# Kernel optimization log

Hardware: AMD Instinct MI355X
Metric: run time of the kernel (lower is better)

Reference implementation:

```python
import jax, jax.numpy as jnp
import numpy as np

B, L, D, H = 2, 2048, 1024, 16
HD = D // H


def setup_inputs() -> dict:
    key = jax.random.key(0)
    ks = jax.random.split(key, 14)
    s = 0.02
    return {
        "hidden_states": jax.random.normal(ks[0], (B, L, D), jnp.float32),
        "position_embeddings": jax.random.normal(ks[1], (B, L, D), jnp.float32),
        "Wcq": jax.random.normal(ks[2], (D, D), jnp.float32) * s,
        "bcq": jnp.zeros((D,), jnp.float32),
        "Wck": jax.random.normal(ks[3], (D, D), jnp.float32) * s,
        "bck": jnp.zeros((D,), jnp.float32),
        "Wpq": jax.random.normal(ks[4], (D, D), jnp.float32) * s,
        "bpq": jnp.zeros((D,), jnp.float32),
        "Wpk": jax.random.normal(ks[5], (D, D), jnp.float32) * s,
        "bpk": jnp.zeros((D,), jnp.float32),
        "rel_bias": jnp.zeros((1, H, 1, 1), jnp.float32),
        "Wo": jax.random.normal(ks[6], (D, D), jnp.float32) * s,
        "bo": jnp.zeros((D,), jnp.float32),
    }


def _split_heads(x):
    # [B, L, D] -> [B, H, L, HD]
    b, l, _ = x.shape
    return x.reshape(b, l, H, HD).transpose(0, 2, 1, 3)


def reference(hidden_states, position_embeddings, Wcq, bcq, Wck, bck,
              Wpq, bpq, Wpk, bpk, rel_bias, Wo, bo):
    cq = _split_heads(hidden_states @ Wcq + bcq)
    ck = _split_heads(hidden_states @ Wck + bck)
    # NOTE: original code (faithfully reproduced) uses content_key as the value
    cv = ck
    pq = _split_heads(position_embeddings @ Wpq + bpq)
    pk = _split_heads(position_embeddings @ Wpk + bpk)

    scores = (jnp.einsum("bhqd,bhkd->bhqk", cq, ck)
              + jnp.einsum("bhqd,bhkd->bhqk", pq, pk)
              + rel_bias)
    attn_weights = jax.nn.softmax(scores / jnp.sqrt(jnp.float32(HD)), axis=-1)
    ctx = jnp.einsum("bhqk,bhkd->bhqd", attn_weights, cv)
    ctx = ctx.transpose(0, 2, 1, 3).reshape(hidden_states.shape[0], -1, D)
    output = ctx @ Wo + bo
    return output, attn_weights
```

## Files before the change

kernel.cpp:

```cpp
#include <hip/hip_runtime.h>
#include <hip/hip_bf16.h>
#include <math.h>


#define Bc 2
#define Lc 2048
#define Dc 1024
#define Hc 16
#define Mc (Bc*Lc)
#define NT 32

typedef __attribute__((ext_vector_type(8))) __bf16 bf16x8;
typedef __attribute__((ext_vector_type(4))) float f32x4;
typedef __attribute__((ext_vector_type(16))) float f32x16;
typedef __attribute__((ext_vector_type(2))) unsigned u32x2;

union U4 { unsigned u[4]; bf16x8 v; };

__device__ __forceinline__ void gl_lds16(const void* g, void* l) {
    __builtin_amdgcn_global_load_lds(
        (const __attribute__((address_space(1))) void*)g,
        (__attribute__((address_space(3))) void*)l, 16, 0, 0);
}
__device__ __forceinline__ unsigned pkbf(float a, float b) {
    unsigned short ua = __builtin_bit_cast(unsigned short, (__bf16)a);
    unsigned short ub = __builtin_bit_cast(unsigned short, (__bf16)b);
    return (unsigned)ua | ((unsigned)ub << 16);
}
__device__ __forceinline__ float lo2f(unsigned u){ return __builtin_bit_cast(float, u << 16); }
__device__ __forceinline__ float hi2f(unsigned u){ return __builtin_bit_cast(float, u & 0xffff0000u); }
#define E2(x) __builtin_amdgcn_exp2f(x)

#define WAIT_VM0  asm volatile("s_waitcnt vmcnt(0)" ::: "memory")
#define WAIT_VM4  asm volatile("s_waitcnt vmcnt(4)" ::: "memory")
#define WAIT_VM8  asm volatile("s_waitcnt vmcnt(8)" ::: "memory")
#define WAIT_VM12 asm volatile("s_waitcnt vmcnt(12)" ::: "memory")
#define WAIT_LG0  asm volatile("s_waitcnt lgkmcnt(0)" ::: "memory")
#define SBAR __builtin_amdgcn_sched_barrier(0)
#define BARRIER do { __builtin_amdgcn_sched_barrier(0); __builtin_amdgcn_s_barrier(); __builtin_amdgcn_sched_barrier(0); } while (0)

__global__ __launch_bounds__(256) void prep_kernel(
    const float* __restrict__ Wcq, const float* __restrict__ Wck,
    const float* __restrict__ Wpq, const float* __restrict__ Wpk,
    const float* __restrict__ Wo,
    __bf16* __restrict__ Wt, __bf16* __restrict__ Woh, __bf16* __restrict__ Wol)
{
    const int z = blockIdx.z;
    const float* W = (z==0)?Wcq:(z==1)?Wck:(z==2)?Wpq:(z==3)?Wpk:Wo;
    const int t = threadIdx.x;
    const int n  = blockIdx.x*64 + (t & 63);
    const int k0 = blockIdx.y*128 + (t >> 6)*32;
    float v[32];
    #pragma unroll
    for (int j = 0; j < 32; ++j) v[j] = W[(size_t)(k0+j)*Dc + n];
    if (z < 4) {
        __bf16* dst = Wt + (size_t)z*Dc*Dc + (size_t)n*Dc + k0;
        #pragma unroll
        for (int c = 0; c < 4; ++c) {
            bf16x8 o;
            #pragma unroll
            for (int j = 0; j < 8; ++j) o[j] = (__bf16)v[c*8+j];
            *(bf16x8*)(dst + c*8) = o;
        }
    } else {
        __bf16* dh = Woh + (size_t)n*Dc + k0;
        __bf16* dl = Wol + (size_t)n*Dc + k0;
        #pragma unroll
        for (int c = 0; c < 4; ++c) {
            bf16x8 oh, ol;
            #pragma unroll
            for (int j = 0; j < 8; ++j) {
                float x = v[c*8+j];
                __bf16 hi = (__bf16)x;
                oh[j] = hi; ol[j] = (__bf16)(x - (float)hi);
            }
            *(bf16x8*)(dh + c*8) = oh;
            *(bf16x8*)(dl + c*8) = ol;
        }
    }
}

__global__ __launch_bounds__(256) void proj_kernel(
    const float* __restrict__ hidden, const float* __restrict__ pos,
    const __bf16* __restrict__ Wt,
    const float* __restrict__ bcq, const float* __restrict__ bck,
    const float* __restrict__ bpq, const float* __restrict__ bpk,
    __bf16* __restrict__ Qc, __bf16* __restrict__ Kc)
{
    const int g = blockIdx.x;
    const int nblk = g >> 7, sg = g & 127, mblk = sg & 31, z = sg >> 5;
    const int m0 = mblk*128, n0 = nblk*128;
    const float* X = (z < 2) ? hidden : pos;
    const __bf16* Wz = Wt + (size_t)z*Dc*Dc;
    const float* bias = (z==0)?bcq:(z==1)?bck:(z==2)?bpq:bpk;
    __bf16* dst = (z & 1) ? Kc : Qc;
    const int half = z >> 1;
    const float scale = (z & 1) ? 1.0f : 0.18033688011112042f;

    const int t = threadIdx.x, lane = t & 63, w = t >> 6;
    const int wm = w >> 1, wn = w & 1;

    __shared__ __align__(16) float  Asf[128][32];
    __shared__ __align__(16) __bf16 Bs[128][32];

    const int arowL = lane >> 3;
    const int acol  = ((lane & 7) ^ arowL) * 4;
    const int brow4 = lane >> 2;
    const int bcol  = ((lane & 3) ^ (brow4 & 3)) * 8;

    f32x4 acc[4][4] = {};

    for (int k0 = 0; k0 < Dc; k0 += 32) {
        #pragma unroll
        for (int i = 0; i < 4; ++i) {
            int row = 8*(4*w+i) + arowL;
            gl_lds16(X + (size_t)(m0+row)*Dc + k0 + acol, (char*)Asf + (4*w+i)*1024);
        }
        #pragma unroll
        for (int i = 0; i < 2; ++i) {
            int row = 16*(2*w+i) + brow4;
            gl_lds16(Wz + (size_t)(n0+row)*Dc + k0 + bcol, (char*)Bs + (2*w+i)*1024);
        }
        WAIT_VM0; __syncthreads();
        bf16x8 a[4], b[4];
        const int s2 = lane >> 4;
        #pragma unroll
        for (int i = 0; i < 4; ++i) {
            int R = wm*64 + i*16 + (lane&15);
            f32x4 x0 = *(const f32x4*)((const char*)&Asf[R][0] + (((2*s2  ) ^ (R&7))*16));
            f32x4 x1 = *(const f32x4*)((const char*)&Asf[R][0] + (((2*s2+1) ^ (R&7))*16));
            bf16x8 af;
            af[0]=(__bf16)x0[0]; af[1]=(__bf16)x0[1]; af[2]=(__bf16)x0[2]; af[3]=(__bf16)x0[3];
            af[4]=(__bf16)x1[0]; af[5]=(__bf16)x1[1]; af[6]=(__bf16)x1[2]; af[7]=(__bf16)x1[3];
            a[i] = af;
            int Rb = wn*64 + i*16 + (lane&15);
            b[i] = *(const bf16x8*)((const char*)&Bs[Rb][0] + ((s2 ^ (Rb&3))*16));
        }
        #pragma unroll
        for (int mi = 0; mi < 4; ++mi)
            #pragma unroll
            for (int ni = 0; ni < 4; ++ni)
                acc[mi][ni] = __builtin_amdgcn_mfma_f32_16x16x32_bf16(a[mi], b[ni], acc[mi][ni], 0, 0, 0);
        __syncthreads();
    }
    #pragma unroll
    for (int mi = 0; mi < 4; ++mi)
        #pragma unroll
        for (int ni = 0; ni < 4; ++ni)
            #pragma unroll
            for (int r = 0; r < 4; ++r) {
                int row = m0 + wm*64 + mi*16 + (lane>>4)*4 + r;
                int col = n0 + wn*64 + ni*16 + (lane&15);
                float v = (acc[mi][ni][r] + bias[col]) * scale;
                int bb = row >> 11, l = row & (Lc-1);
                int hh = col >> 6,  hd = col & 63;
                dst[(((size_t)bb*Hc + hh)*Lc + l)*128 + half*64 + hd] = (__bf16)v;
            }
}

__global__ __launch_bounds__(256) void vt_kernel(
    const __bf16* __restrict__ Kc, __bf16* __restrict__ VT)
{
    const int l0 = blockIdx.x * 128, hb = blockIdx.y;
    const int t = threadIdx.x, w = t >> 6, lane = t & 63;
    __shared__ __bf16 T[128][72];
    const __bf16* src = Kc + ((size_t)hb*Lc + l0)*128;
    {
        const int lr = t >> 3, cc = t & 7;
        #pragma unroll
        for (int j = 0; j < 4; ++j)
            *(bf16x8*)&T[lr + j*32][cc*8] = *(const bf16x8*)(src + (size_t)(lr + j*32)*128 + cc*8);
    }
    __syncthreads();
    {
        const int d = lane;
        __bf16* dstp = VT + ((size_t)hb*64 + d)*Lc + l0 + w*32;
        #pragma unroll
        for (int j = 0; j < 4; ++j) {
            bf16x8 o;
            #pragma unroll
            for (int i = 0; i < 8; ++i) o[i] = T[w*32 + j*8 + i][d];
            *(bf16x8*)(dstp + j*8) = o;
        }
    }
}

__global__ __launch_bounds__(256, 2) void attn1_kernel(
    const __bf16* __restrict__ Qc, const __bf16* __restrict__ Kc,
    const float* __restrict__ rel_bias, float* __restrict__ baddp)
{
    const int g = blockIdx.x;
    const int qt = g >> 5, hb = g & 31, h = hb & 15;
    const int q0 = qt * 128;
    const int t = threadIdx.x, lane = t & 63, w = t >> 6;
    const int ln31 = lane & 31, hi = lane >> 5;

    const __bf16* Qp = Qc + (size_t)hb * Lc * 128;
    const __bf16* Kp = Kc + (size_t)hb * Lc * 128;

    __shared__ __align__(16) char smem[49152];

    bf16x8 qa[8];
    {
        const __bf16* qrow = Qp + (size_t)(q0 + w*32 + ln31) * 128 + hi*8;
        #pragma unroll
        for (int ks = 0; ks < 8; ++ks) qa[ks] = *(const bf16x8*)(qrow + ks*16);
    }

    int kof[4];
    #pragma unroll
    for (int c = 0; c < 4; ++c) {
        int rl = c*4 + (lane >> 4);
        int rr = w*16 + rl;
        kof[c] = rr*128 + (((lane & 15) ^ rl) * 8);
    }
    int kR[8];
    #pragma unroll
    for (int ks = 0; ks < 8; ++ks) kR[ks] = ((ks*2 + hi) ^ (lane & 15)) * 8;

    #define STAGE_K(B, KT) do { \
        const __bf16* kb_ = Kp + (size_t)(KT)*8192; \
        gl_lds16(kb_ + kof[0], smem + ((B)*64 + w*16 +  0)*256); \
        gl_lds16(kb_ + kof[1], smem + ((B)*64 + w*16 +  4)*256); \
        gl_lds16(kb_ + kof[2], smem + ((B)*64 + w*16 +  8)*256); \
        gl_lds16(kb_ + kof[3], smem + ((B)*64 + w*16 + 12)*256); \
    } while (0)
    #define KB(B, ROW, KS) (*(const bf16x8*)(smem + ((B)*64 + (ROW))*256 + kR[KS]*2))

    const float bc = rel_bias[h] * 0.18033688011112042f;
    float lp[4] = {0.f, 0.f, 0.f, 0.f};

    STAGE_K(0, 0); STAGE_K(1, 1);
    WAIT_VM4; BARRIER;
    for (int kt = 0; kt < NT; ++kt) {
        if (kt+2 < NT) STAGE_K((kt+2) % 3, kt+2);
        SBAR;
        const int buf = kt % 3;
        f32x16 s0, s1;
        #pragma unroll
        for (int r = 0; r < 16; ++r) { s0[r] = bc; s1[r] = bc; }
        __builtin_amdgcn_s_setprio(1);
        #pragma unroll
        for (int ks = 0; ks < 8; ++ks) {
            bf16x8 kb0 = KB(buf, ln31, ks);
            bf16x8 kb1 = KB(buf, 32 + ln31, ks);
            s0 = __builtin_amdgcn_mfma_f32_32x32x16_bf16(kb0, qa[ks], s0, 0, 0, 0);
            s1 = __builtin_amdgcn_mfma_f32_32x32x16_bf16(kb1, qa[ks], s1, 0, 0, 0);
        }
        __builtin_amdgcn_s_setprio(0);
        #pragma unroll
        for (int r = 0; r < 16; ++r) {
            lp[r & 3] += E2(s0[r]);
            lp[r & 3] += E2(s1[r]);
        }
        if (kt+2 < NT) { WAIT_VM4; } else { WAIT_VM0; }
        BARRIER;
    }
    float lsum = (lp[0] + lp[1]) + (lp[2] + lp[3]);
    lsum += __shfl_xor(lsum, 32);
    if (!hi) baddp[(size_t)hb*Lc + q0 + w*32 + ln31] = bc - log2f(lsum);
    #undef STAGE_K
    #undef KB
}

__global__ __launch_bounds__(256, 2) void attn2_kernel(
    const __bf16* __restrict__ Qc, const __bf16* __restrict__ Kc,
    const __bf16* __restrict__ VT, const float* __restrict__ baddp,
    float* __restrict__ attn, __bf16* __restrict__ ctxh)
{
    const int g = blockIdx.x;
    const int qt = g >> 5, hb = g & 31, h = hb & 15, bb = hb >> 4;
    const int q0 = qt * 128;
    const int t = threadIdx.x, lane = t & 63, w = t >> 6;
    const int ln31 = lane & 31, hi = lane >> 5;

    const __bf16* Qp = Qc + (size_t)hb * Lc * 128;
    const __bf16* Kp = Kc + (size_t)hb * Lc * 128;
    const __bf16* Vp = VT + (size_t)hb * 64 * Lc;

    __shared__ __align__(16) char smem[81920];
    char* const VsB = smem + 49152;
    char* const PsW = smem + 65536 + w*4096;

    bf16x8 qa[8];
    {
        const __bf16* qrow = Qp + (size_t)(q0 + w*32 + ln31) * 128 + hi*8;
        #pragma unroll
        for (int ks = 0; ks < 8; ++ks) qa[ks] = *(const bf16x8*)(qrow + ks*16);
    }
    const float badd = baddp[(size_t)hb*Lc + q0 + w*32 + ln31];

    int kof[4];
    #pragma unroll
    for (int c = 0; c < 4; ++c) {
        int rl = c*4 + (lane >> 4);
        int rr = w*16 + rl;
        kof[c] = rr*128 + (((lane & 15) ^ rl) * 8);
    }
    int vof[2];
    #pragma unroll
    for (int c = 0; c < 2; ++c) {
        int dl = lane >> 3;
        int dd = w*16 + c*8 + dl;
        vof[c] = dd*2048 + (((lane & 7) ^ dl) * 8);
    }
    int kR[8];
    #pragma unroll
    for (int ks = 0; ks < 8; ++ks) kR[ks] = ((ks*2 + hi) ^ (lane & 15)) * 8;
    int vR[4];
    #pragma unroll
    for (int ks = 0; ks < 4; ++ks) vR[ks] = ((ks*2 + hi) ^ (lane & 7)) * 8;

    #define STAGE_K(B, KT) do { \
        const __bf16* kb_ = Kp + (size_t)(KT)*8192; \
        gl_lds16(kb_ + kof[0], smem + ((B)*64 + w*16 +  0)*256); \
        gl_lds16(kb_ + kof[1], smem + ((B)*64 + w*16 +  4)*256); \
        gl_lds16(kb_ + kof[2], smem + ((B)*64 + w*16 +  8)*256); \
        gl_lds16(kb_ + kof[3], smem + ((B)*64 + w*16 + 12)*256); \
    } while (0)
    #define STAGE_V(B, KT) do { \
        const __bf16* vb_ = Vp + (KT)*64; \
        gl_lds16(vb_ + vof[0], VsB + ((B)*64 + w*16 + 0)*128); \
        gl_lds16(vb_ + vof[1], VsB + ((B)*64 + w*16 + 8)*128); \
    } while (0)
    #define KB(B, ROW, KS) (*(const bf16x8*)(smem + ((B)*64 + (ROW))*256 + kR[KS]*2))
    #define VB(B, ROW, KS) (*(const bf16x8*)(VsB  + ((B)*64 + (ROW))*128 + vR[KS]*2))

    f32x16 ctx0 = {}, ctx1 = {};
    float* abase = attn + ((size_t)hb*Lc + q0 + w*32)*Lc;
    const int rr2 = lane >> 4;
    const int s8  = lane & 15;

    STAGE_K(0, 0); STAGE_V(0, 0); STAGE_K(1, 1);
    WAIT_VM4; BARRIER;

    for (int kt = 0; kt < NT; ++kt) {
        if (kt+1 < NT) STAGE_V((kt+1) & 1, kt+1);
        if (kt+2 < NT) STAGE_K((kt+2) % 3, kt+2);
        SBAR;
        const int buf = kt % 3;
        f32x16 s0, s1;
        #pragma unroll
        for (int r = 0; r < 16; ++r) { s0[r] = badd; s1[r] = badd; }
        __builtin_amdgcn_s_setprio(1);
        #pragma unroll
        for (int ks = 0; ks < 8; ++ks) {
            bf16x8 kb0 = KB(buf, ln31, ks);
            bf16x8 kb1 = KB(buf, 32 + ln31, ks);
            s0 = __builtin_amdgcn_mfma_f32_32x32x16_bf16(kb0, qa[ks], s0, 0, 0, 0);
            s1 = __builtin_amdgcn_mfma_f32_32x32x16_bf16(kb1, qa[ks], s1, 0, 0, 0);
        }
        __builtin_amdgcn_s_setprio(0);
        unsigned u0[8], u1[8], r0[8], r1[8];
        #pragma unroll
        for (int gq = 0; gq < 4; ++gq) {
            u0[gq]   = pkbf(E2(s0[4*gq+0]), E2(s0[4*gq+1]));
            u1[gq]   = pkbf(E2(s0[4*gq+2]), E2(s0[4*gq+3]));
            u0[4+gq] = pkbf(E2(s1[4*gq+0]), E2(s1[4*gq+1]));
            u1[4+gq] = pkbf(E2(s1[4*gq+2]), E2(s1[4*gq+3]));
        }
        #pragma unroll
        for (int gq = 0; gq < 8; ++gq) {
            r0[gq] = __shfl_xor(u0[gq], 32);
            r1[gq] = __shfl_xor(u1[gq], 32);
        }
        bf16x8 pb[4];
        #pragma unroll
        for (int ks = 0; ks < 4; ++ks) {
            const int gq = 2*ks + hi;
            U4 u;
            u.u[0] = hi ? r0[gq] : u0[gq];
            u.u[1] = hi ? r1[gq] : u1[gq];
            u.u[2] = hi ? u0[gq] : r0[gq];
            u.u[3] = hi ? u1[gq] : r1[gq];
            pb[ks] = u.v;
            *(bf16x8*)(PsW + ln31*128 + ((gq ^ (ln31 & 7))*16)) = u.v;
        }
        __builtin_amdgcn_s_setprio(1);
        #pragma unroll
        for (int ks = 0; ks < 4; ++ks) {
            bf16x8 v0 = VB(kt & 1, ln31, ks);
            bf16x8 v1 = VB(kt & 1, 32 + ln31, ks);
            ctx0 = __builtin_amdgcn_mfma_f32_32x32x16_bf16(pb[ks], v0, ctx0, 0, 0, 0);
            ctx1 = __builtin_amdgcn_mfma_f32_32x32x16_bf16(pb[ks], v1, ctx1, 0, 0, 0);
        }
        __builtin_amdgcn_s_setprio(0);
        WAIT_LG0; SBAR;
        #pragma unroll
        for (int j = 0; j < 8; ++j) {
            const int row = j*4 + rr2;
            u32x2 d = *(const u32x2*)(PsW + row*128 + (((s8>>1) ^ (row&7))*16) + (s8&1)*8);
            f32x4 o;
            o[0]=lo2f(d[0]); o[1]=hi2f(d[0]); o[2]=lo2f(d[1]); o[3]=hi2f(d[1]);
            __builtin_nontemporal_store(o, (f32x4*)(abase + (size_t)row*Lc + kt*64 + s8*4));
        }
        if (kt+1 < NT) {
            if (kt+2 < NT) { WAIT_VM12; } else { WAIT_VM8; }
            BARRIER;
        }
    }

    #pragma unroll
    for (int r = 0; r < 16; ++r) {
        const int R = (r&3) + 8*(r>>2) + 4*hi;
        const size_t row = (size_t)bb*Lc + q0 + w*32 + R;
        ctxh[row*Dc + h*64 + ln31]      = (__bf16)ctx0[r];
        ctxh[row*Dc + h*64 + 32 + ln31] = (__bf16)ctx1[r];
    }
    #undef STAGE_K
    #undef STAGE_V
    #undef KB
    #undef VB
}

__global__ __launch_bounds__(256) void out_kernel(
    const __bf16* __restrict__ ctxh, const __bf16* __restrict__ Woh,
    const __bf16* __restrict__ Wol, const float* __restrict__ bo,
    float* __restrict__ out)
{
    const int m0 = blockIdx.y * 128, n0 = blockIdx.x * 128;
    const int t = threadIdx.x, lane = t & 63, w = t >> 6;
    const int wm = w >> 1, wn = w & 1;

    __shared__ __align__(16) __bf16 As[128][32];
    __shared__ __align__(16) __bf16 Bh[128][32];
    __shared__ __align__(16) __bf16 Bl[128][32];

    const int row4 = lane >> 2;
    const int scol = ((lane & 3) ^ (row4 & 3)) * 8;

    f32x4 acc[4][4] = {};

    for (int k0 = 0; k0 < Dc; k0 += 32) {
        #pragma unroll
        for (int i = 0; i < 2; ++i) {
            int row = 16*(2*w+i) + row4;
            gl_lds16(ctxh + (size_t)(m0+row)*Dc + k0 + scol, (char*)As + (2*w+i)*1024);
            gl_lds16(Woh  + (size_t)(n0+row)*Dc + k0 + scol, (char*)Bh + (2*w+i)*1024);
            gl_lds16(Wol  + (size_t)(n0+row)*Dc + k0 + scol, (char*)Bl + (2*w+i)*1024);
        }
        WAIT_VM0; __syncthreads();
        bf16x8 a[4], bh[4], bl[4];
        const int s2 = lane >> 4;
        #pragma unroll
        for (int i = 0; i < 4; ++i) {
            int Ra = wm*64 + i*16 + (lane&15);
            int Rb = wn*64 + i*16 + (lane&15);
            a[i]  = *(const bf16x8*)((const char*)&As[Ra][0] + ((s2 ^ (Ra&3))*16));
            bh[i] = *(const bf16x8*)((const char*)&Bh[Rb][0] + ((s2 ^ (Rb&3))*16));
            bl[i] = *(const bf16x8*)((const char*)&Bl[Rb][0] + ((s2 ^ (Rb&3))*16));
        }
        #pragma unroll
        for (int mi = 0; mi < 4; ++mi)
            #pragma unroll
            for (int ni = 0; ni < 4; ++ni) {
                acc[mi][ni] = __builtin_amdgcn_mfma_f32_16x16x32_bf16(a[mi], bh[ni], acc[mi][ni], 0, 0, 0);
                acc[mi][ni] = __builtin_amdgcn_mfma_f32_16x16x32_bf16(a[mi], bl[ni], acc[mi][ni], 0, 0, 0);
            }
        __syncthreads();
    }
    #pragma unroll
    for (int mi = 0; mi < 4; ++mi)
        #pragma unroll
        for (int ni = 0; ni < 4; ++ni)
            #pragma unroll
            for (int r = 0; r < 4; ++r) {
                int row = m0 + wm*64 + mi*16 + (lane>>4)*4 + r;
                int col = n0 + wn*64 + ni*16 + (lane&15);
                __builtin_nontemporal_store(acc[mi][ni][r] + bo[col],
                                            out + (size_t)row * Dc + col);
            }
}

extern "C" void kernel_launch(void* const* d_in, const int* in_sizes, int n_in,
                              void* d_out, int out_size, void* d_ws, size_t ws_size,
                              hipStream_t stream)
{
    const float* hidden = (const float*)d_in[0];
    const float* pos    = (const float*)d_in[1];
    const float* Wcq = (const float*)d_in[2];  const float* bcq = (const float*)d_in[3];
    const float* Wck = (const float*)d_in[4];  const float* bck = (const float*)d_in[5];
    const float* Wpq = (const float*)d_in[6];  const float* bpq = (const float*)d_in[7];
    const float* Wpk = (const float*)d_in[8];  const float* bpk = (const float*)d_in[9];
    const float* relb = (const float*)d_in[10];
    const float* Wo  = (const float*)d_in[11]; const float* bo  = (const float*)d_in[12];

    float* out  = (float*)d_out;
    float* attn = out + (size_t)Mc * Dc;

    __bf16* ws   = (__bf16*)d_ws;
    __bf16* Woh  = ws;
    __bf16* Wol  = ws + (1u<<20);
    __bf16* Wt   = ws + (2u<<20);
    __bf16* ctxh = Wt;
    __bf16* Qc   = ws + (6u<<20);
    __bf16* Kc   = ws + (14u<<20);
    __bf16* VTb  = ws + (22u<<20);
    float*  badd = (float*)(ws + (26u<<20));

    prep_kernel<<<dim3(16, 8, 5), 256, 0, stream>>>(Wcq, Wck, Wpq, Wpk, Wo, Wt, Woh, Wol);
    proj_kernel<<<dim3(1024), 256, 0, stream>>>(hidden, pos, Wt, bcq, bck, bpq, bpk, Qc, Kc);
    vt_kernel<<<dim3(Lc/128, 32), 256, 0, stream>>>(Kc, VTb);
    attn1_kernel<<<dim3(512), 256, 0, stream>>>(Qc, Kc, relb, badd);
    attn2_kernel<<<dim3(512), 256, 0, stream>>>(Qc, Kc, VTb, badd, attn, ctxh);
    out_kernel<<<dim3(8, 32), 256, 0, stream>>>(ctxh, Woh, Wol, bo, out);
}
```

Measured before the change: 326.4 us.

## Pre-convert activations to bf16 and use MFMA-fragment-ordered LDS layouts

The prep kernel gains extra z-slices that convert hidden and position inputs to bf16 once, written into the attention-output buffer as scratch. The projection GEMM then loads bf16 A tiles instead of fp32 and no longer converts in the inner loop. The projection, attention and output kernels all switch their LDS staging to a fragment-major layout, where each lane reads a contiguous 16 bytes at lane*16, replacing XOR-swizzled addressing. The GEMM K-step also grows from 32 to 64. This aims to cut global traffic, conversion work and LDS address math, at the cost of an extra pass over the inputs and more LDS per block.

Result: slower. 357.8 us (+9.6%).

```diff
diff --git a/kernel.cpp b/kernel.cpp
--- a/kernel.cpp
+++ b/kernel.cpp
@@ -40,14 +40,32 @@
 #define BARRIER do { __builtin_amdgcn_sched_barrier(0); __builtin_amdgcn_s_barrier(); __builtin_amdgcn_sched_barrier(0); } while (0)
 
 __global__ __launch_bounds__(256) void prep_kernel(
+    const float* __restrict__ hidden, const float* __restrict__ pos,
     const float* __restrict__ Wcq, const float* __restrict__ Wck,
     const float* __restrict__ Wpq, const float* __restrict__ Wpk,
     const float* __restrict__ Wo,
-    __bf16* __restrict__ Wt, __bf16* __restrict__ Woh, __bf16* __restrict__ Wol)
+    __bf16* __restrict__ Wt, __bf16* __restrict__ Woh, __bf16* __restrict__ Wol,
+    __bf16* __restrict__ Xh, __bf16* __restrict__ Xp)
 {
     const int z = blockIdx.z;
+    const int t = threadIdx.x;
+    if (z >= 5) {
+        const float* X = (z==5) ? hidden : pos;
+        __bf16* dst    = (z==5) ? Xh : Xp;
+        const size_t base = ((size_t)(blockIdx.y*16 + blockIdx.x)*256 + t) * 128;
+        #pragma unroll
+        for (int c = 0; c < 16; ++c) {
+            const float* sp = X + base + c*8;
+            float4 v0 = *(const float4*)sp;
+            float4 v1 = *(const float4*)(sp + 4);
+            bf16x8 o;
+            o[0]=(__bf16)v0.x; o[1]=(__bf16)v0.y; o[2]=(__bf16)v0.z; o[3]=(__bf16)v0.w;
+            o[4]=(__bf16)v1.x; o[5]=(__bf16)v1.y; o[6]=(__bf16)v1.z; o[7]=(__bf16)v1.w;
+            *(bf16x8*)(dst + base + c*8) = o;
+        }
+        return;
+    }
     const float* W = (z==0)?Wcq:(z==1)?Wck:(z==2)?Wpq:(z==3)?Wpk:Wo;
-    const int t = threadIdx.x;
     const int n  = blockIdx.x*64 + (t & 63);
     const int k0 = blockIdx.y*128 + (t >> 6)*32;
     float v[32];
@@ -81,7 +99,7 @@
 }
 
 __global__ __launch_bounds__(256) void proj_kernel(
-    const float* __restrict__ hidden, const float* __restrict__ pos,
+    const __bf16* __restrict__ Xh, const __bf16* __restrict__ Xp,
     const __bf16* __restrict__ Wt,
     const float* __restrict__ bcq, const float* __restrict__ bck,
     const float* __restrict__ bpq, const float* __restrict__ bpk,
@@ -90,7 +108,7 @@
     const int g = blockIdx.x;
     const int nblk = g >> 7, sg = g & 127, mblk = sg & 31, z = sg >> 5;
     const int m0 = mblk*128, n0 = nblk*128;
-    const float* X = (z < 2) ? hidden : pos;
+    const __bf16* X = (z < 2) ? Xh : Xp;
     const __bf16* Wz = Wt + (size_t)z*Dc*Dc;
     const float* bias = (z==0)?bcq:(z==1)?bck:(z==2)?bpq:bpk;
     __bf16* dst = (z & 1) ? Kc : Qc;
@@ -100,47 +118,36 @@
     const int t = threadIdx.x, lane = t & 63, w = t >> 6;
     const int wm = w >> 1, wn = w & 1;
 
-    __shared__ __align__(16) float  Asf[128][32];
-    __shared__ __align__(16) __bf16 Bs[128][32];
-
-    const int arowL = lane >> 3;
-    const int acol  = ((lane & 7) ^ arowL) * 4;
-    const int brow4 = lane >> 2;
-    const int bcol  = ((lane & 3) ^ (brow4 & 3)) * 8;
+    __shared__ __align__(16) char smem[32768];
 
     f32x4 acc[4][4] = {};
 
-    for (int k0 = 0; k0 < Dc; k0 += 32) {
-        #pragma unroll
-        for (int i = 0; i < 4; ++i) {
-            int row = 8*(4*w+i) + arowL;
-            gl_lds16(X + (size_t)(m0+row)*Dc + k0 + acol, (char*)Asf + (4*w+i)*1024);
-        }
-        #pragma unroll
-        for (int i = 0; i < 2; ++i) {
-            int row = 16*(2*w+i) + brow4;
-            gl_lds16(Wz + (size_t)(n0+row)*Dc + k0 + bcol, (char*)Bs + (2*w+i)*1024);
+    for (int k0 = 0; k0 < Dc; k0 += 64) {
+        #pragma unroll
+        for (int c = 0; c < 4; ++c) {
+            const int d = w*4 + c;
+            const int h = d >> 3, i = (d >> 1) & 3, kk = d & 1;
+            const int rr = h*64 + i*16 + (lane & 15);
+            const int kc = k0 + kk*32 + (lane >> 4)*8;
+            gl_lds16(X  + (size_t)(m0 + rr)*Dc + kc, smem + d*1024);
+            gl_lds16(Wz + (size_t)(n0 + rr)*Dc + kc, smem + 16384 + d*1024);
         }
         WAIT_VM0; __syncthreads();
-        bf16x8 a[4], b[4];
-        const int s2 = lane >> 4;
-        #pragma unroll
-        for (int i = 0; i < 4; ++i) {
-            int R = wm*64 + i*16 + (lane&15);
-            f32x4 x0 = *(const f32x4*)((const char*)&Asf[R][0] + (((2*s2  ) ^ (R&7))*16));
-            f32x4 x1 = *(const f32x4*)((const char*)&Asf[R][0] + (((2*s2+1) ^ (R&7))*16));
-            bf16x8 af;
-            af[0]=(__bf16)x0[0]; af[1]=(__bf16)x0[1]; af[2]=(__bf16)x0[2]; af[3]=(__bf16)x0[3];
-            af[4]=(__bf16)x1[0]; af[5]=(__bf16)x1[1]; af[6]=(__bf16)x1[2]; af[7]=(__bf16)x1[3];
-            a[i] = af;
-            int Rb = wn*64 + i*16 + (lane&15);
-            b[i] = *(const bf16x8*)((const char*)&Bs[Rb][0] + ((s2 ^ (Rb&3))*16));
-        }
+        bf16x8 a[4][2], b[4][2];
+        #pragma unroll
+        for (int i = 0; i < 4; ++i)
+            #pragma unroll
+            for (int kk = 0; kk < 2; ++kk) {
+                a[i][kk] = *(const bf16x8*)(smem + (wm*8 + i*2 + kk)*1024 + lane*16);
+                b[i][kk] = *(const bf16x8*)(smem + 16384 + (wn*8 + i*2 + kk)*1024 + lane*16);
+            }
         #pragma unroll
         for (int mi = 0; mi < 4; ++mi)
             #pragma unroll
-            for (int ni = 0; ni < 4; ++ni)
-                acc[mi][ni] = __builtin_amdgcn_mfma_f32_16x16x32_bf16(a[mi], b[ni], acc[mi][ni], 0, 0, 0);
+            for (int ni = 0; ni < 4; ++ni) {
+                acc[mi][ni] = __builtin_amdgcn_mfma_f32_16x16x32_bf16(a[mi][0], b[ni][0], acc[mi][ni], 0, 0, 0);
+                acc[mi][ni] = __builtin_amdgcn_mfma_f32_16x16x32_bf16(a[mi][1], b[ni][1], acc[mi][ni], 0, 0, 0);
+            }
         __syncthreads();
     }
     #pragma unroll
@@ -207,25 +214,18 @@
         for (int ks = 0; ks < 8; ++ks) qa[ks] = *(const bf16x8*)(qrow + ks*16);
     }
 
-    int kof[4];
-    #pragma unroll
-    for (int c = 0; c < 4; ++c) {
-        int rl = c*4 + (lane >> 4);
-        int rr = w*16 + rl;
-        kof[c] = rr*128 + (((lane & 15) ^ rl) * 8);
-    }
-    int kR[8];
-    #pragma unroll
-    for (int ks = 0; ks < 8; ++ks) kR[ks] = ((ks*2 + hi) ^ (lane & 15)) * 8;
-
     #define STAGE_K(B, KT) do { \
         const __bf16* kb_ = Kp + (size_t)(KT)*8192; \
-        gl_lds16(kb_ + kof[0], smem + ((B)*64 + w*16 +  0)*256); \
-        gl_lds16(kb_ + kof[1], smem + ((B)*64 + w*16 +  4)*256); \
-        gl_lds16(kb_ + kof[2], smem + ((B)*64 + w*16 +  8)*256); \
-        gl_lds16(kb_ + kof[3], smem + ((B)*64 + w*16 + 12)*256); \
+        _Pragma("unroll") \
+        for (int c = 0; c < 4; ++c) { \
+            const int d = w*4 + c; \
+            const int hf = d >> 3, ks = d & 7; \
+            gl_lds16(kb_ + (size_t)(hf*32 + ln31)*128 + ks*16 + hi*8, \
+                     smem + (B)*16384 + d*1024); \
+        } \
     } while (0)
-    #define KB(B, ROW, KS) (*(const bf16x8*)(smem + ((B)*64 + (ROW))*256 + kR[KS]*2))
+    #define KB0(B, KS) (*(const bf16x8*)(smem + (B)*16384 + (KS)*1024 + lane*16))
+    #define KB1(B, KS) (*(const bf16x8*)(smem + (B)*16384 + (8+(KS))*1024 + lane*16))
 
     const float bc = rel_bias[h] * 0.18033688011112042f;
     float lp[4] = {0.f, 0.f, 0.f, 0.f};
@@ -242,8 +242,8 @@
         __builtin_amdgcn_s_setprio(1);
         #pragma unroll
         for (int ks = 0; ks < 8; ++ks) {
-            bf16x8 kb0 = KB(buf, ln31, ks);
-            bf16x8 kb1 = KB(buf, 32 + ln31, ks);
+            bf16x8 kb0 = KB0(buf, ks);
+            bf16x8 kb1 = KB1(buf, ks);
             s0 = __builtin_amdgcn_mfma_f32_32x32x16_bf16(kb0, qa[ks], s0, 0, 0, 0);
             s1 = __builtin_amdgcn_mfma_f32_32x32x16_bf16(kb1, qa[ks], s1, 0, 0, 0);
         }
@@ -260,7 +260,8 @@
     lsum += __shfl_xor(lsum, 32);
     if (!hi) baddp[(size_t)hb*Lc + q0 + w*32 + ln31] = bc - log2f(lsum);
     #undef STAGE_K
-    #undef KB
+    #undef KB0
+    #undef KB1
 }
 
 __global__ __launch_bounds__(256, 2) void attn2_kernel(
@@ -290,41 +291,30 @@
     }
     const float badd = baddp[(size_t)hb*Lc + q0 + w*32 + ln31];
 
-    int kof[4];
-    #pragma unroll
-    for (int c = 0; c < 4; ++c) {
-        int rl = c*4 + (lane >> 4);
-        int rr = w*16 + rl;
-        kof[c] = rr*128 + (((lane & 15) ^ rl) * 8);
-    }
-    int vof[2];
-    #pragma unroll
-    for (int c = 0; c < 2; ++c) {
-        int dl = lane >> 3;
-        int dd = w*16 + c*8 + dl;
-        vof[c] = dd*2048 + (((lane & 7) ^ dl) * 8);
-    }
-    int kR[8];
-    #pragma unroll
-    for (int ks = 0; ks < 8; ++ks) kR[ks] = ((ks*2 + hi) ^ (lane & 15)) * 8;
-    int vR[4];
-    #pragma unroll
-    for (int ks = 0; ks < 4; ++ks) vR[ks] = ((ks*2 + hi) ^ (lane & 7)) * 8;
-
     #define STAGE_K(B, KT) do { \
         const __bf16* kb_ = Kp + (size_t)(KT)*8192; \
-        gl_lds16(kb_ + kof[0], smem + ((B)*64 + w*16 +  0)*256); \
-        gl_lds16(kb_ + kof[1], smem + ((B)*64 + w*16 +  4)*256); \
-        gl_lds16(kb_ + kof[2], smem + ((B)*64 + w*16 +  8)*256); \
-        gl_lds16(kb_ + kof[3], smem + ((B)*64 + w*16 + 12)*256); \
+        _Pragma("unroll") \
+        for (int c = 0; c < 4; ++c) { \
+            const int d = w*4 + c; \
+            const int hf = d >> 3, ks = d & 7; \
+            gl_lds16(kb_ + (size_t)(hf*32 + ln31)*128 + ks*16 + hi*8, \
+                     smem + (B)*16384 + d*1024); \
+        } \
     } while (0)
     #define STAGE_V(B, KT) do { \
         const __bf16* vb_ = Vp + (KT)*64; \
-        gl_lds16(vb_ + vof[0], VsB + ((B)*64 + w*16 + 0)*128); \
-        gl_lds16(vb_ + vof[1], VsB + ((B)*64 + w*16 + 8)*128); \
+        _Pragma("unroll") \
+        for (int c = 0; c < 2; ++c) { \
+            const int d = w*2 + c; \
+            const int hf = d >> 2, ks = d & 3; \
+            gl_lds16(vb_ + (size_t)(hf*32 + ln31)*2048 + ks*16 + hi*8, \
+                     VsB + (B)*8192 + d*1024); \
+        } \
     } while (0)
-    #define KB(B, ROW, KS) (*(const bf16x8*)(smem + ((B)*64 + (ROW))*256 + kR[KS]*2))
-    #define VB(B, ROW, KS) (*(const bf16x8*)(VsB  + ((B)*64 + (ROW))*128 + vR[KS]*2))
+    #define KB0(B, KS) (*(const bf16x8*)(smem + (B)*16384 + (KS)*1024 + lane*16))
+    #define KB1(B, KS) (*(const bf16x8*)(smem + (B)*16384 + (8+(KS))*1024 + lane*16))
+    #define VB0(B, KS) (*(const bf16x8*)(VsB + (B)*8192 + (KS)*1024 + lane*16))
+    #define VB1(B, KS) (*(const bf16x8*)(VsB + (B)*8192 + (4+(KS))*1024 + lane*16))
 
     f32x16 ctx0 = {}, ctx1 = {};
     float* abase = attn + ((size_t)hb*Lc + q0 + w*32)*Lc;
@@ -345,8 +335,8 @@
         __builtin_amdgcn_s_setprio(1);
         #pragma unroll
         for (int ks = 0; ks < 8; ++ks) {
-            bf16x8 kb0 = KB(buf, ln31, ks);
-            bf16x8 kb1 = KB(buf, 32 + ln31, ks);
+            bf16x8 kb0 = KB0(buf, ks);
+            bf16x8 kb1 = KB1(buf, ks);
             s0 = __builtin_amdgcn_mfma_f32_32x32x16_bf16(kb0, qa[ks], s0, 0, 0, 0);
             s1 = __builtin_amdgcn_mfma_f32_32x32x16_bf16(kb1, qa[ks], s1, 0, 0, 0);
         }
@@ -379,8 +369,8 @@
         __builtin_amdgcn_s_setprio(1);
         #pragma unroll
         for (int ks = 0; ks < 4; ++ks) {
-            bf16x8 v0 = VB(kt & 1, ln31, ks);
-            bf16x8 v1 = VB(kt & 1, 32 + ln31, ks);
+            bf16x8 v0 = VB0(kt & 1, ks);
+            bf16x8 v1 = VB1(kt & 1, ks);
             ctx0 = __builtin_amdgcn_mfma_f32_32x32x16_bf16(pb[ks], v0, ctx0, 0, 0, 0);
             ctx1 = __builtin_amdgcn_mfma_f32_32x32x16_bf16(pb[ks], v1, ctx1, 0, 0, 0);
         }
@@ -409,8 +399,10 @@
     }
     #undef STAGE_K
     #undef STAGE_V
-    #undef KB
-    #undef VB
+    #undef KB0
+    #undef KB1
+    #undef VB0
+    #undef VB1
 }
 
 __global__ __launch_bounds__(256) void out_kernel(
@@ -422,40 +414,39 @@
     const int t = threadIdx.x, lane = t & 63, w = t >> 6;
     const int wm = w >> 1, wn = w & 1;
 
-    __shared__ __align__(16) __bf16 As[128][32];
-    __shared__ __align__(16) __bf16 Bh[128][32];
-    __shared__ __align__(16) __bf16 Bl[128][32];
-
-    const int row4 = lane >> 2;
-    const int scol = ((lane & 3) ^ (row4 & 3)) * 8;
+    __shared__ __align__(16) char smem[49152];
 
     f32x4 acc[4][4] = {};
 
-    for (int k0 = 0; k0 < Dc; k0 += 32) {
-        #pragma unroll
-        for (int i = 0; i < 2; ++i) {
-            int row = 16*(2*w+i) + row4;
-            gl_lds16(ctxh + (size_t)(m0+row)*Dc + k0 + scol, (char*)As + (2*w+i)*1024);
-            gl_lds16(Woh  + (size_t)(n0+row)*Dc + k0 + scol, (char*)Bh + (2*w+i)*1024);
-            gl_lds16(Wol  + (size_t)(n0+row)*Dc + k0 + scol, (char*)Bl + (2*w+i)*1024);
+    for (int k0 = 0; k0 < Dc; k0 += 64) {
+        #pragma unroll
+        for (int c = 0; c < 4; ++c) {
+            const int d = w*4 + c;
+            const int h = d >> 3, i = (d >> 1) & 3, kk = d & 1;
+            const int rr = h*64 + i*16 + (lane & 15);
+            const int kc = k0 + kk*32 + (lane >> 4)*8;
+            gl_lds16(ctxh + (size_t)(m0 + rr)*Dc + kc, smem + d*1024);
+            gl_lds16(Woh  + (size_t)(n0 + rr)*Dc + kc, smem + 16384 + d*1024);
+            gl_lds16(Wol  + (size_t)(n0 + rr)*Dc + kc, smem + 32768 + d*1024);
         }
         WAIT_VM0; __syncthreads();
-        bf16x8 a[4], bh[4], bl[4];
-        const int s2 = lane >> 4;
-        #pragma unroll
-        for (int i = 0; i < 4; ++i) {
-            int Ra = wm*64 + i*16 + (lane&15);
-            int Rb = wn*64 + i*16 + (lane&15);
-            a[i]  = *(const bf16x8*)((const char*)&As[Ra][0] + ((s2 ^ (Ra&3))*16));
-            bh[i] = *(const bf16x8*)((const char*)&Bh[Rb][0] + ((s2 ^ (Rb&3))*16));
-            bl[i] = *(const bf16x8*)((const char*)&Bl[Rb][0] + ((s2 ^ (Rb&3))*16));
-        }
+        bf16x8 a[4][2], bh[4][2], bl[4][2];
+        #pragma unroll
+        for (int i = 0; i < 4; ++i)
+            #pragma unroll
+            for (int kk = 0; kk < 2; ++kk) {
+                a[i][kk]  = *(const bf16x8*)(smem + (wm*8 + i*2 + kk)*1024 + lane*16);
+                bh[i][kk] = *(const bf16x8*)(smem + 16384 + (wn*8 + i*2 + kk)*1024 + lane*16);
+                bl[i][kk] = *(const bf16x8*)(smem + 32768 + (wn*8 + i*2 + kk)*1024 + lane*16);
+            }
         #pragma unroll
         for (int mi = 0; mi < 4; ++mi)
             #pragma unroll
             for (int ni = 0; ni < 4; ++ni) {
-                acc[mi][ni] = __builtin_amdgcn_mfma_f32_16x16x32_bf16(a[mi], bh[ni], acc[mi][ni], 0, 0, 0);
-                acc[mi][ni] = __builtin_amdgcn_mfma_f32_16x16x32_bf16(a[mi], bl[ni], acc[mi][ni], 0, 0, 0);
+                acc[mi][ni] = __builtin_amdgcn_mfma_f32_16x16x32_bf16(a[mi][0], bh[ni][0], acc[mi][ni], 0, 0, 0);
+                acc[mi][ni] = __builtin_amdgcn_mfma_f32_16x16x32_bf16(a[mi][0], bl[ni][0], acc[mi][ni], 0, 0, 0);
+                acc[mi][ni] = __builtin_amdgcn_mfma_f32_16x16x32_bf16(a[mi][1], bh[ni][1], acc[mi][ni], 0, 0, 0);
+                acc[mi][ni] = __builtin_amdgcn_mfma_f32_16x16x32_bf16(a[mi][1], bl[ni][1], acc[mi][ni], 0, 0, 0);
             }
         __syncthreads();
     }
@@ -498,8 +489,12 @@
     __bf16* VTb  = ws + (22u<<20);
     float*  badd = (float*)(ws + (26u<<20));
 
-    prep_kernel<<<dim3(16, 8, 5), 256, 0, stream>>>(Wcq, Wck, Wpq, Wpk, Wo, Wt, Woh, Wol);
-    proj_kernel<<<dim3(1024), 256, 0, stream>>>(hidden, pos, Wt, bcq, bck, bpq, bpk, Qc, Kc);
+    __bf16* Xh = (__bf16*)attn;
+    __bf16* Xp = Xh + (4u<<20);
+
+    prep_kernel<<<dim3(16, 8, 7), 256, 0, stream>>>(
+        hidden, pos, Wcq, Wck, Wpq, Wpk, Wo, Wt, Woh, Wol, Xh, Xp);
+    proj_kernel<<<dim3(1024), 256, 0, stream>>>(Xh, Xp, Wt, bcq, bck, bpq, bpk, Qc, Kc);
     vt_kernel<<<dim3(Lc/128, 32), 256, 0, stream>>>(Kc, VTb);
     attn1_kernel<<<dim3(512), 256, 0, stream>>>(Qc, Kc, relb, badd);
     attn2_kernel<<<dim3(512), 256, 0, stream>>>(Qc, Kc, VTb, badd, attn, ctxh);
```
